# Optimization experiments

Hardware: AMD Instinct MI355X
Metric: run time of the kernel (lower is better)

## Reference

```python
import jax, jax.numpy as jnp
import numpy as np

N = 50000      # nodes
E = 800000     # edges (avg degree 16)
DIN = 64       # input feature dim
DOUT = 64      # output feature dim
NSLOPE = 0.2   # LeakyReLU negative slope


def setup_inputs() -> dict:
    key = jax.random.key(0)
    k1, k2, k3, k4 = jax.random.split(key, 4)
    x = jax.random.normal(k1, (N, DIN), dtype=jnp.float32)
    W = jax.random.normal(k2, (DOUT, DIN), dtype=jnp.float32) * (1.0 / np.sqrt(DIN))
    b = jnp.zeros((DOUT,), dtype=jnp.float32)
    a = jax.random.normal(k3, (DOUT,), dtype=jnp.float32) * (1.0 / np.sqrt(DOUT))
    edge_index = jax.random.randint(k4, (2, E), 0, N, dtype=jnp.int32)
    return {"x": x, "W": W, "b": b, "a": a, "edge_index": edge_index}


def reference(x, W, b, a, edge_index):
    # GATv2: e_ij = a^T LeakyReLU(W h_i + W h_j + b); softmax over incoming
    # neighbors j of node i; h_i' = sigmoid(sum_j alpha_ij * W h_j)
    Wh = x @ W.T + b                          # [N, DOUT]
    src, dst = edge_index[0], edge_index[1]   # edge j -> i
    s = Wh[dst] + Wh[src]                     # [E, DOUT] per-edge pre-activation
    e = jnp.where(s > 0, s, NSLOPE * s) @ a   # [E] attention logits
    # numerically stable segment softmax over destination nodes
    emax = jax.ops.segment_max(e, dst, num_segments=N)       # [N]
    emax = jnp.where(jnp.isfinite(emax), emax, 0.0)          # nodes with no edges
    ex = jnp.exp(e - emax[dst])                               # [E]
    denom = jax.ops.segment_sum(ex, dst, num_segments=N)      # [N]
    alpha = ex / jnp.maximum(denom[dst], 1e-9)                # [E]
    agg = jax.ops.segment_sum(alpha[:, None] * Wh[src], dst, num_segments=N)
    return jax.nn.sigmoid(agg)                # [N, DOUT]
```

## Files before the change

### kernel.cpp

```cpp
#include <hip/hip_runtime.h>
#include <hip/hip_bf16.h>
#include <math.h>

#define NN 50000
#define EE 800000
#define DD 64
#define NSLOPE 0.2f
#define NBUCK 196
#define CAP 4608
#define CHUNK 2048
#define BINB ((EE + CHUNK - 1) / CHUNK)
#define WHB 782

__device__ __forceinline__ float leaky(float s) { return s > 0.f ? s : NSLOPE * s; }
__device__ __forceinline__ float b2f(unsigned short u) {
    return __uint_as_float(((unsigned)u) << 16);
}
__device__ __forceinline__ unsigned short f2b(float f) {
    unsigned b = __float_as_uint(f);
    return (unsigned short)((b + 0x7fffu + ((b >> 16) & 1u)) >> 16);
}

__global__ void __launch_bounds__(256) bin_kernel(
    const int* __restrict__ ei, unsigned int* __restrict__ gbuf,
    int* __restrict__ gCursor) {
    __shared__ int cnt[256];
    __shared__ int excl[256];
    __shared__ int cur[256];
    __shared__ int base[256];
    __shared__ unsigned int pairs[CHUNK];
    int tid = threadIdx.x;
    int start = blockIdx.x * CHUNK;
    int nedge = min(CHUNK, EE - start);
    cnt[tid] = 0; cur[tid] = 0;
    __syncthreads();
    for (int j = 0; j < CHUNK / 256; ++j) {
        int i = start + tid + j * 256;
        if (i < EE) atomicAdd(&cnt[((unsigned int)ei[EE + i]) >> 8], 1);
    }
    __syncthreads();
    int v = cnt[tid];
    excl[tid] = v; __syncthreads();
    for (int o = 1; o < 256; o <<= 1) {
        int t = (tid >= o) ? excl[tid - o] : 0;
        __syncthreads();
        excl[tid] += t;
        __syncthreads();
    }
    int ex = excl[tid] - v;
    __syncthreads();
    excl[tid] = ex;
    __syncthreads();
    for (int j = 0; j < CHUNK / 256; ++j) {
        int i = start + tid + j * 256;
        if (i < EE) {
            unsigned int src = (unsigned int)ei[i];
            unsigned int dst = (unsigned int)ei[EE + i];
            int b = dst >> 8;
            int r = atomicAdd(&cur[b], 1);
            pairs[excl[b] + r] = (dst << 16) | src;
        }
    }
    if (tid < NBUCK) base[tid] = atomicAdd(&gCursor[tid], cnt[tid]);
    __syncthreads();
    for (int i = tid; i < nedge; i += 256) {
        unsigned int p = pairs[i];
        int b = p >> 24;
        gbuf[(size_t)b * CAP + base[b] + (i - excl[b])] = p;
    }
}

__global__ void __launch_bounds__(256) csr_wh_kernel(
    const unsigned int* __restrict__ gbuf, const int* __restrict__ gCursor,
    int* __restrict__ off, unsigned short* __restrict__ csr,
    const float* __restrict__ x, const float* __restrict__ W,
    const float* __restrict__ bias, float* __restrict__ Wh,
    unsigned short* __restrict__ Whb) {
    __shared__ __align__(16) char smem[20480];
    int tid = threadIdx.x;

    if (blockIdx.x < NBUCK) {
        int* s    = (int*)smem;
        int* hist = s + 256;
        int* excl = s + 512;
        int* cur  = s + 768;
        int k = blockIdx.x;
        int v = (tid < NBUCK) ? gCursor[tid] : 0;
        s[tid] = v; __syncthreads();
        for (int o = 1; o < 256; o <<= 1) {
            int t = (tid >= o) ? s[tid - o] : 0;
            __syncthreads();
            s[tid] += t;
            __syncthreads();
        }
        int base_k = (k == 0) ? 0 : s[k - 1];
        int cnt = s[k] - base_k;
        const unsigned int* bp = gbuf + (size_t)k * CAP;
        hist[tid] = 0; cur[tid] = 0;
        __syncthreads();
        for (int i = tid; i < cnt; i += 256)
            atomicAdd(&hist[(bp[i] >> 16) & 255], 1);
        __syncthreads();
        int hv = hist[tid];
        excl[tid] = hv; __syncthreads();
        for (int o = 1; o < 256; o <<= 1) {
            int t = (tid >= o) ? excl[tid - o] : 0;
            __syncthreads();
            excl[tid] += t;
            __syncthreads();
        }
        int hex = excl[tid] - hv;
        __syncthreads();
        excl[tid] = hex;
        __syncthreads();
        int dst = k * 256 + tid;
        if (dst < NN) off[dst] = base_k + hex;
        if (k == 0 && tid == 0) off[NN] = EE;
        for (int i = tid; i < cnt; i += 256) {
            unsigned int p = bp[i];
            int local = (p >> 16) & 255;
            int slot = base_k + excl[local] + atomicAdd(&cur[local], 1);
            csr[slot] = (unsigned short)(p & 0xffffu);
        }
        return;
    }

    int bid = blockIdx.x - NBUCK;
    float4* Wl = (float4*)smem;
    float4 (*xr)[4][16] = (float4 (*)[4][16])(smem + 16384);
    const float4* W4 = (const float4*)W;
    const float4* x4 = (const float4*)x;
    for (int i = tid; i < 1024; i += 256) {
        int c = i >> 4, k4 = i & 15;
        Wl[c * 16 + (k4 ^ (c & 15))] = W4[i];
    }
    __syncthreads();
    int wv = tid >> 6, lane = tid & 63;
    int c = lane;
    float4 wreg[16];
#pragma unroll
    for (int k4 = 0; k4 < 16; ++k4) wreg[k4] = Wl[c * 16 + (k4 ^ (c & 15))];
    float bv = bias[c];
    int l16 = lane >> 4, q = lane & 15;
    for (int rowbase = (bid * 4 + wv) * 4; rowbase < NN; rowbase += WHB * 16) {
        xr[wv][l16][q] = x4[(size_t)(rowbase + l16) * 16 + q];
        float acc0 = bv, acc1 = bv, acc2 = bv, acc3 = bv;
#pragma unroll
        for (int k4 = 0; k4 < 16; ++k4) {
            float4 w  = wreg[k4];
            float4 q0 = xr[wv][0][k4];
            float4 q1 = xr[wv][1][k4];
            float4 q2 = xr[wv][2][k4];
            float4 q3 = xr[wv][3][k4];
            acc0 += w.x * q0.x + w.y * q0.y + w.z * q0.z + w.w * q0.w;
            acc1 += w.x * q1.x + w.y * q1.y + w.z * q1.z + w.w * q1.w;
            acc2 += w.x * q2.x + w.y * q2.y + w.z * q2.z + w.w * q2.w;
            acc3 += w.x * q3.x + w.y * q3.y + w.z * q3.z + w.w * q3.w;
        }
        Wh[(size_t)(rowbase + 0) * DD + c] = acc0;
        Wh[(size_t)(rowbase + 1) * DD + c] = acc1;
        Wh[(size_t)(rowbase + 2) * DD + c] = acc2;
        Wh[(size_t)(rowbase + 3) * DD + c] = acc3;
        Whb[(size_t)(rowbase + 0) * DD + c] = f2b(acc0);
        Whb[(size_t)(rowbase + 1) * DD + c] = f2b(acc1);
        Whb[(size_t)(rowbase + 2) * DD + c] = f2b(acc2);
        Whb[(size_t)(rowbase + 3) * DD + c] = f2b(acc3);
    }
}

__global__ void __launch_bounds__(256) fused_kernel(
    const float4* __restrict__ Wh4, const unsigned short* __restrict__ Whb,
    const float4* __restrict__ a4, const int* __restrict__ off,
    const unsigned short* __restrict__ csr, float4* __restrict__ out4) {
    int wave = threadIdx.x >> 6, lane = threadIdx.x & 63;
    int node = blockIdx.x * 4 + wave;
    int b = lane >> 4, f4 = lane & 15;
    float4 av  = a4[f4];
    float4 whi = Wh4[(size_t)node * 16 + f4];
    int beg = off[node], end = off[node + 1];
    float den = 0.f;
    float4 acc = make_float4(0.f, 0.f, 0.f, 0.f);
    if (beg < end) {
        int last = end - 1;
        int i0 = min(beg + b, last);
        int i1 = min(beg + 4 + b, last);
        ushort4 p0 = *(const ushort4*)(Whb + (size_t)csr[i0] * DD + f4 * 4);
        ushort4 p1 = *(const ushort4*)(Whb + (size_t)csr[i1] * DD + f4 * 4);
        for (int base = beg; base < end; base += 4) {
            ushort4 u = p0;
            p0 = p1;
            int ni = min(base + 8 + b, last);
            p1 = *(const ushort4*)(Whb + (size_t)csr[ni] * DD + f4 * 4);
            float4 whs = make_float4(b2f(u.x), b2f(u.y), b2f(u.z), b2f(u.w));
            float t = av.x * leaky(whi.x + whs.x) + av.y * leaky(whi.y + whs.y)
                    + av.z * leaky(whi.z + whs.z) + av.w * leaky(whi.w + whs.w);
            t += __shfl_xor(t, 1, 64);
            t += __shfl_xor(t, 2, 64);
            t += __shfl_xor(t, 4, 64);
            t += __shfl_xor(t, 8, 64);
            float ex = (base + b < end) ? __expf(t) : 0.f;
            den += ex;
            acc.x += ex * whs.x; acc.y += ex * whs.y;
            acc.z += ex * whs.z; acc.w += ex * whs.w;
        }
    }
    acc.x += __shfl_xor(acc.x, 16, 64); acc.y += __shfl_xor(acc.y, 16, 64);
    acc.z += __shfl_xor(acc.z, 16, 64); acc.w += __shfl_xor(acc.w, 16, 64);
    den   += __shfl_xor(den,   16, 64);
    acc.x += __shfl_xor(acc.x, 32, 64); acc.y += __shfl_xor(acc.y, 32, 64);
    acc.z += __shfl_xor(acc.z, 32, 64); acc.w += __shfl_xor(acc.w, 32, 64);
    den   += __shfl_xor(den,   32, 64);
    if (b == 0) {
        float id = 1.f / fmaxf(den, 1e-9f);
        float4 o;
        o.x = 1.f / (1.f + __expf(-acc.x * id));
        o.y = 1.f / (1.f + __expf(-acc.y * id));
        o.z = 1.f / (1.f + __expf(-acc.z * id));
        o.w = 1.f / (1.f + __expf(-acc.w * id));
        out4[(size_t)node * 16 + f4] = o;
    }
}

extern "C" void kernel_launch(void* const* d_in, const int* in_sizes, int n_in,
                              void* d_out, int out_size, void* d_ws, size_t ws_size,
                              hipStream_t stream) {
    const float* x = (const float*)d_in[0];
    const float* W = (const float*)d_in[1];
    const float* b = (const float*)d_in[2];
    const float* a = (const float*)d_in[3];
    const int*   ei = (const int*)d_in[4];
    float* out = (float*)d_out;

    char* ws = (char*)d_ws;
    float*          Wh      = (float*)(ws);
    int*            gCursor = (int*)(ws + 12800000);
    int*            off     = (int*)(ws + 12801024);
    unsigned int*   gbuf    = (unsigned int*)(ws + 13001216);
    unsigned short* csr     = (unsigned short*)(ws + 16613888);
    unsigned short* Whb     = (unsigned short*)(ws + 18214912);

    hipMemsetAsync(gCursor, 0, 1024, stream);
    bin_kernel<<<BINB, 256, 0, stream>>>(ei, gbuf, gCursor);
    csr_wh_kernel<<<NBUCK + WHB, 256, 0, stream>>>(gbuf, gCursor, off, csr,
                                                   x, W, b, Wh, Whb);
    fused_kernel<<<NN / 4, 256, 0, stream>>>((const float4*)Wh, Whb,
                                             (const float4*)a, off, csr,
                                             (float4*)out);
}
```

Before: 139.1 us.

## Drop fp32 Wh buffer and process 8 edges per wave with 16-byte loads

The fp32 copy of Wh is no longer written or read, so the destination node's own features now come from the bf16 copy. This removes about 12.8 MB of writes and the matching reads. The aggregation kernel is remapped to 8 edges per wave iteration with 8 features per lane, using uint4 loads of bf16 features. That makes each gather wider and shortens the shuffle reduction for the attention logit. The trade-offs are slightly lower precision for the self term and higher register use per lane.

Result: faster. 131.3 us (-5.6%).

```diff
diff --git a/kernel.cpp b/kernel.cpp
--- a/kernel.cpp
+++ b/kernel.cpp
@@ -13,12 +13,13 @@
 #define WHB 782
 
 __device__ __forceinline__ float leaky(float s) { return s > 0.f ? s : NSLOPE * s; }
-__device__ __forceinline__ float b2f(unsigned short u) {
-    return __uint_as_float(((unsigned)u) << 16);
-}
 __device__ __forceinline__ unsigned short f2b(float f) {
     unsigned b = __float_as_uint(f);
     return (unsigned short)((b + 0x7fffu + ((b >> 16) & 1u)) >> 16);
+}
+__device__ __forceinline__ void unpack2(unsigned u, float& lo, float& hi) {
+    lo = __uint_as_float(u << 16);
+    hi = __uint_as_float(u & 0xffff0000u);
 }
 
 __global__ void __launch_bounds__(256) bin_kernel(
@@ -74,8 +75,7 @@
     const unsigned int* __restrict__ gbuf, const int* __restrict__ gCursor,
     int* __restrict__ off, unsigned short* __restrict__ csr,
     const float* __restrict__ x, const float* __restrict__ W,
-    const float* __restrict__ bias, float* __restrict__ Wh,
-    unsigned short* __restrict__ Whb) {
+    const float* __restrict__ bias, unsigned short* __restrict__ Whb) {
     __shared__ __align__(16) char smem[20480];
     int tid = threadIdx.x;
 
@@ -157,10 +157,6 @@
             acc2 += w.x * q2.x + w.y * q2.y + w.z * q2.z + w.w * q2.w;
             acc3 += w.x * q3.x + w.y * q3.y + w.z * q3.z + w.w * q3.w;
         }
-        Wh[(size_t)(rowbase + 0) * DD + c] = acc0;
-        Wh[(size_t)(rowbase + 1) * DD + c] = acc1;
-        Wh[(size_t)(rowbase + 2) * DD + c] = acc2;
-        Wh[(size_t)(rowbase + 3) * DD + c] = acc3;
         Whb[(size_t)(rowbase + 0) * DD + c] = f2b(acc0);
         Whb[(size_t)(rowbase + 1) * DD + c] = f2b(acc1);
         Whb[(size_t)(rowbase + 2) * DD + c] = f2b(acc2);
@@ -169,55 +165,66 @@
 }
 
 __global__ void __launch_bounds__(256) fused_kernel(
-    const float4* __restrict__ Wh4, const unsigned short* __restrict__ Whb,
-    const float4* __restrict__ a4, const int* __restrict__ off,
-    const unsigned short* __restrict__ csr, float4* __restrict__ out4) {
+    const unsigned short* __restrict__ Whb, const float4* __restrict__ a4,
+    const int* __restrict__ off, const unsigned short* __restrict__ csr,
+    float4* __restrict__ out4) {
     int wave = threadIdx.x >> 6, lane = threadIdx.x & 63;
     int node = blockIdx.x * 4 + wave;
-    int b = lane >> 4, f4 = lane & 15;
-    float4 av  = a4[f4];
-    float4 whi = Wh4[(size_t)node * 16 + f4];
+    int eb = lane >> 3, fq = lane & 7;
+    float4 a0 = a4[fq * 2], a1 = a4[fq * 2 + 1];
+    float av[8] = {a0.x, a0.y, a0.z, a0.w, a1.x, a1.y, a1.z, a1.w};
+    uint4 wu = *(const uint4*)(Whb + (size_t)node * DD + fq * 8);
+    float whi[8];
+    unpack2(wu.x, whi[0], whi[1]); unpack2(wu.y, whi[2], whi[3]);
+    unpack2(wu.z, whi[4], whi[5]); unpack2(wu.w, whi[6], whi[7]);
     int beg = off[node], end = off[node + 1];
     float den = 0.f;
-    float4 acc = make_float4(0.f, 0.f, 0.f, 0.f);
+    float acc[8] = {0.f, 0.f, 0.f, 0.f, 0.f, 0.f, 0.f, 0.f};
     if (beg < end) {
         int last = end - 1;
-        int i0 = min(beg + b, last);
-        int i1 = min(beg + 4 + b, last);
-        ushort4 p0 = *(const ushort4*)(Whb + (size_t)csr[i0] * DD + f4 * 4);
-        ushort4 p1 = *(const ushort4*)(Whb + (size_t)csr[i1] * DD + f4 * 4);
-        for (int base = beg; base < end; base += 4) {
-            ushort4 u = p0;
+        int i0 = min(beg + eb, last);
+        int i1 = min(beg + 8 + eb, last);
+        uint4 p0 = *(const uint4*)(Whb + (size_t)csr[i0] * DD + fq * 8);
+        uint4 p1 = *(const uint4*)(Whb + (size_t)csr[i1] * DD + fq * 8);
+        for (int base = beg; base < end; base += 8) {
+            uint4 u = p0;
             p0 = p1;
-            int ni = min(base + 8 + b, last);
-            p1 = *(const ushort4*)(Whb + (size_t)csr[ni] * DD + f4 * 4);
-            float4 whs = make_float4(b2f(u.x), b2f(u.y), b2f(u.z), b2f(u.w));
-            float t = av.x * leaky(whi.x + whs.x) + av.y * leaky(whi.y + whs.y)
-                    + av.z * leaky(whi.z + whs.z) + av.w * leaky(whi.w + whs.w);
+            int ni = min(base + 16 + eb, last);
+            p1 = *(const uint4*)(Whb + (size_t)csr[ni] * DD + fq * 8);
+            float whs[8];
+            unpack2(u.x, whs[0], whs[1]); unpack2(u.y, whs[2], whs[3]);
+            unpack2(u.z, whs[4], whs[5]); unpack2(u.w, whs[6], whs[7]);
+            float t = 0.f;
+#pragma unroll
+            for (int j = 0; j < 8; ++j) t += av[j] * leaky(whi[j] + whs[j]);
             t += __shfl_xor(t, 1, 64);
             t += __shfl_xor(t, 2, 64);
             t += __shfl_xor(t, 4, 64);
-            t += __shfl_xor(t, 8, 64);
-            float ex = (base + b < end) ? __expf(t) : 0.f;
+            float ex = (base + eb < end) ? __expf(t) : 0.f;
             den += ex;
-            acc.x += ex * whs.x; acc.y += ex * whs.y;
-            acc.z += ex * whs.z; acc.w += ex * whs.w;
-        }
-    }
-    acc.x += __shfl_xor(acc.x, 16, 64); acc.y += __shfl_xor(acc.y, 16, 64);
-    acc.z += __shfl_xor(acc.z, 16, 64); acc.w += __shfl_xor(acc.w, 16, 64);
-    den   += __shfl_xor(den,   16, 64);
-    acc.x += __shfl_xor(acc.x, 32, 64); acc.y += __shfl_xor(acc.y, 32, 64);
-    acc.z += __shfl_xor(acc.z, 32, 64); acc.w += __shfl_xor(acc.w, 32, 64);
-    den   += __shfl_xor(den,   32, 64);
-    if (b == 0) {
+#pragma unroll
+            for (int j = 0; j < 8; ++j) acc[j] += ex * whs[j];
+        }
+    }
+#pragma unroll
+    for (int o = 8; o <= 32; o <<= 1) {
+        den += __shfl_xor(den, o, 64);
+#pragma unroll
+        for (int j = 0; j < 8; ++j) acc[j] += __shfl_xor(acc[j], o, 64);
+    }
+    if (eb == 0) {
         float id = 1.f / fmaxf(den, 1e-9f);
-        float4 o;
-        o.x = 1.f / (1.f + __expf(-acc.x * id));
-        o.y = 1.f / (1.f + __expf(-acc.y * id));
-        o.z = 1.f / (1.f + __expf(-acc.z * id));
-        o.w = 1.f / (1.f + __expf(-acc.w * id));
-        out4[(size_t)node * 16 + f4] = o;
+        float4 o0, o1;
+        o0.x = 1.f / (1.f + __expf(-acc[0] * id));
+        o0.y = 1.f / (1.f + __expf(-acc[1] * id));
+        o0.z = 1.f / (1.f + __expf(-acc[2] * id));
+        o0.w = 1.f / (1.f + __expf(-acc[3] * id));
+        o1.x = 1.f / (1.f + __expf(-acc[4] * id));
+        o1.y = 1.f / (1.f + __expf(-acc[5] * id));
+        o1.z = 1.f / (1.f + __expf(-acc[6] * id));
+        o1.w = 1.f / (1.f + __expf(-acc[7] * id));
+        out4[(size_t)node * 16 + fq * 2]     = o0;
+        out4[(size_t)node * 16 + fq * 2 + 1] = o1;
     }
 }
 
@@ -232,18 +239,16 @@
     float* out = (float*)d_out;
 
     char* ws = (char*)d_ws;
-    float*          Wh      = (float*)(ws);
-    int*            gCursor = (int*)(ws + 12800000);
-    int*            off     = (int*)(ws + 12801024);
-    unsigned int*   gbuf    = (unsigned int*)(ws + 13001216);
-    unsigned short* csr     = (unsigned short*)(ws + 16613888);
-    unsigned short* Whb     = (unsigned short*)(ws + 18214912);
+    unsigned short* Whb     = (unsigned short*)(ws);
+    int*            gCursor = (int*)(ws + 6400000);
+    int*            off     = (int*)(ws + 6401024);
+    unsigned int*   gbuf    = (unsigned int*)(ws + 6601216);
+    unsigned short* csr     = (unsigned short*)(ws + 10213888);
 
     hipMemsetAsync(gCursor, 0, 1024, stream);
     bin_kernel<<<BINB, 256, 0, stream>>>(ei, gbuf, gCursor);
     csr_wh_kernel<<<NBUCK + WHB, 256, 0, stream>>>(gbuf, gCursor, off, csr,
-                                                   x, W, b, Wh, Whb);
-    fused_kernel<<<NN / 4, 256, 0, stream>>>((const float4*)Wh, Whb,
-                                             (const float4*)a, off, csr,
+                                                   x, W, b, Whb);
+    fused_kernel<<<NN / 4, 256, 0, stream>>>(Whb, (const float4*)a, off, csr,
                                              (float4*)out);
 }
```
